# Kernel tuning notes

Hardware: AMD Instinct MI355X
Metric: run time of the kernel (lower is better)

The kernel has to match this reference:

```python
import jax, jax.numpy as jnp
import numpy as np

D_IN, D, N_HEADS, K, VOCAB = 768, 512, 8, 6, 1000
HEAD_DIM = D // N_HEADS


def setup_inputs() -> dict:
    key = jax.random.key(0)
    ks = jax.random.split(key, 16)
    B, T, L = 32, 4096, 512
    s = 0.02
    return {
        "video_features": jax.random.normal(ks[0], (B, T, D_IN), jnp.float32),
        "input_ids": jax.random.randint(ks[1], (B, L), 0, VOCAB),
        "attention_mask": jnp.ones((B, L), jnp.float32),
        # video_encoder (Linear 768->512), stored [in, out]
        "W_enc": jax.random.normal(ks[2], (D_IN, D), jnp.float32) * s,
        "b_enc": jnp.zeros((D,), jnp.float32),
        # frame_selector (Linear 512->1)
        "W_sel": jax.random.normal(ks[3], (D, 1), jnp.float32) * s,
        "b_sel": jnp.zeros((1,), jnp.float32),
        # text_encoder embedding
        "emb": jax.random.normal(ks[4], (VOCAB, D), jnp.float32) * s,
        # MultiheadAttention in/out projections
        "W_q": jax.random.normal(ks[5], (D, D), jnp.float32) * s,
        "W_k": jax.random.normal(ks[6], (D, D), jnp.float32) * s,
        "W_v": jax.random.normal(ks[7], (D, D), jnp.float32) * s,
        "b_q": jnp.zeros((D,), jnp.float32),
        "b_k": jnp.zeros((D,), jnp.float32),
        "b_v": jnp.zeros((D,), jnp.float32),
        "W_o": jax.random.normal(ks[8], (D, D), jnp.float32) * s,
        "b_o": jnp.zeros((D,), jnp.float32),
        # classifier (Linear 512->1000)
        "W_cls": jax.random.normal(ks[9], (D, VOCAB), jnp.float32) * s,
        "b_cls": jnp.zeros((VOCAB,), jnp.float32),
    }


def reference(video_features, input_ids, attention_mask, W_enc, b_enc, W_sel,
              b_sel, emb, W_q, W_k, W_v, b_q, b_k, b_v, W_o, b_o, W_cls, b_cls):
    # encode frames: [B, T, 512]
    ve = jax.nn.relu(jnp.einsum('bti,io->bto', video_features, W_enc) + b_enc)
    # frame scores [B, T] -> top-6 gather
    scores = jnp.einsum('btd,do->bto', ve, W_sel)[..., 0] + b_sel[0]
    _, top_idx = jax.lax.top_k(scores, K)                      # [B, K]
    reps = jnp.take_along_axis(ve, top_idx[:, :, None], axis=1)  # [B, K, 512]
    # text embedding (query), reps as key/value
    txt = emb[input_ids]                                       # [B, L, 512]
    B, L, _ = txt.shape
    q = (txt @ W_q + b_q).reshape(B, L, N_HEADS, HEAD_DIM)
    k = (reps @ W_k + b_k).reshape(B, K, N_HEADS, HEAD_DIM)
    v = (reps @ W_v + b_v).reshape(B, K, N_HEADS, HEAD_DIM)
    scale = 1.0 / np.sqrt(HEAD_DIM).astype(np.float32)
    attn = jax.nn.softmax(jnp.einsum('blhd,bkhd->bhlk', q, k) * scale, axis=-1)
    ctx = jnp.einsum('bhlk,bkhd->blhd', attn, v).reshape(B, L, D)
    fused = ctx @ W_o + b_o
    logits = fused @ W_cls + b_cls                             # [B, L, 1000]
    return logits, reps
```

## Files before the change

### kernel.cpp

```cpp
#include <hip/hip_runtime.h>
#include <math.h>


#define DEV __device__ __forceinline__

typedef _Float16 half8 __attribute__((ext_vector_type(8)));
typedef float f32x4v __attribute__((ext_vector_type(4)));

DEV unsigned short f2h_bits(float f) {
  union { _Float16 h; unsigned short u; } cv;
  cv.h = (_Float16)f;
  return cv.u;
}

DEV void gload16(const void* g, void* lds) {
  auto* gp = reinterpret_cast<const __attribute__((address_space(1))) unsigned int*>(
      reinterpret_cast<unsigned long long>(g));
  auto* lp = reinterpret_cast<__attribute__((address_space(3))) unsigned int*>(
      reinterpret_cast<unsigned long long>(lds));
  __builtin_amdgcn_global_load_lds(gp, lp, 16, 0, 0);
}

__global__ __launch_bounds__(256) void prep_k(
    const float* __restrict__ W_enc, unsigned short* __restrict__ WencT,
    const float* __restrict__ emb, const float* __restrict__ W_q,
    const float* __restrict__ b_q, float* __restrict__ Qe,
    const float* __restrict__ W_o, const float* __restrict__ W_cls,
    unsigned short* __restrict__ WocT, const float* __restrict__ b_o,
    const float* __restrict__ b_cls, float* __restrict__ boc) {
  __shared__ float plds[2080];
  const int blk = blockIdx.x, tid = threadIdx.x;
  if (blk < 96) {
    unsigned short* t = (unsigned short*)plds;
    const int k0 = (blk % 12) * 64, n0 = (blk / 12) * 64;
    for (int e = tid; e < 4096; e += 256) {
      int kk = e >> 6, nn = e & 63;
      t[kk * 65 + nn] = f2h_bits(W_enc[(size_t)(k0 + kk) * 512 + n0 + nn]);
    }
    __syncthreads();
    for (int e = tid; e < 4096; e += 256) {
      int nn = e >> 6, kk = e & 63;
      WencT[(size_t)(n0 + nn) * 768 + k0 + kk] = t[kk * 65 + nn];
    }
  } else if (blk < 346) {
    float* er = plds;
    const int r0 = (blk - 96) * 4;
    for (int i = tid; i < 2048; i += 256) er[i] = emb[(size_t)r0 * 512 + i];
    __syncthreads();
    const int j0 = tid, j1 = tid + 256;
    float a0[4], a1[4];
#pragma unroll
    for (int r = 0; r < 4; ++r) { a0[r] = 0.f; a1[r] = 0.f; }
    for (int i = 0; i < 512; ++i) {
      float w0 = W_q[i * 512 + j0], w1 = W_q[i * 512 + j1];
#pragma unroll
      for (int r = 0; r < 4; ++r) {
        a0[r] += er[r * 512 + i] * w0;
        a1[r] += er[r * 512 + i] * w1;
      }
    }
    float bq0 = b_q[j0], bq1 = b_q[j1];
#pragma unroll
    for (int r = 0; r < 4; ++r) {
      Qe[(size_t)(r0 + r) * 512 + j0] = a0[r] + bq0;
      Qe[(size_t)(r0 + r) * 512 + j1] = a1[r] + bq1;
    }
  } else if (blk < 474) {
    float* wr = plds;
    const int i0 = (blk - 346) * 4;
    for (int i = tid; i < 2048; i += 256) wr[i] = W_o[(size_t)i0 * 512 + i];
    __syncthreads();
    float a[4][4];
#pragma unroll
    for (int r = 0; r < 4; ++r)
#pragma unroll
      for (int c = 0; c < 4; ++c) a[r][c] = 0.f;
    for (int m = 0; m < 512; ++m) {
      float wc[4];
#pragma unroll
      for (int c = 0; c < 4; ++c) {
        int j = tid + c * 256;
        wc[c] = (j < 1000) ? W_cls[(size_t)m * 1000 + j] : 0.f;
      }
#pragma unroll
      for (int r = 0; r < 4; ++r) {
        float x = wr[r * 512 + m];
#pragma unroll
        for (int c = 0; c < 4; ++c) a[r][c] += x * wc[c];
      }
    }
#pragma unroll
    for (int r = 0; r < 4; ++r)
#pragma unroll
      for (int c = 0; c < 4; ++c) {
        int j = tid + c * 256;
        if (j < 1000) WocT[(size_t)j * 512 + i0 + r] = f2h_bits(a[r][c]);
      }
    if (blk == 346) {
      for (int i = tid; i < 24 * 512; i += 256) WocT[512000 + i] = 0;
    }
  } else {
    int j = (blk - 474) * 256 + tid;
    float s = 0.f;
    if (j < 1000) {
      for (int m = 0; m < 512; ++m) s += b_o[m] * W_cls[(size_t)m * 1000 + j];
      s += b_cls[j];
    }
    boc[j] = s;
  }
}

__global__ __launch_bounds__(1024, 4) void score_gemm(
    const float* __restrict__ vf, const unsigned short* __restrict__ WencT,
    const float* __restrict__ b_enc, const float* __restrict__ W_sel,
    const float* __restrict__ b_sel, float* __restrict__ scores) {
  __shared__ unsigned short As[2][128 * 32];
  __shared__ unsigned short Bs[2][512 * 32];
  __shared__ float red[16 * 64];

  const int tid = threadIdx.x;
  const int wv = tid >> 6, lane = tid & 63;
  const int quad = lane >> 4, l15 = lane & 15;
  const int wr = wv >> 3, wc = wv & 7;
  const int rowBase = blockIdx.x * 128;
  const int rso = ((quad ^ (l15 & 3)) << 4);
  char* const AsB0 = (char*)As[0];
  char* const AsB1 = (char*)As[1];
  char* const BsB0 = (char*)Bs[0];
  char* const BsB1 = (char*)Bs[1];

  f32x4v acc[4][4];
#pragma unroll
  for (int i = 0; i < 4; ++i)
#pragma unroll
    for (int j = 0; j < 4; ++j) acc[i][j] = (f32x4v){0.f, 0.f, 0.f, 0.f};

  const int arow = tid >> 3, aseg = tid & 7;
  const float* aSrc = vf + (size_t)(rowBase + arow) * 768 + aseg * 4;
  const int aslot = aseg >> 1, ahalf = aseg & 1;
  const int adst = arow * 64 + ((aslot ^ (arow & 3)) << 4) + ahalf * 8;

  auto packA = [&](float4 f, char* An) {
    uint2 pk;
    pk.x = (unsigned int)f2h_bits(f.x) | ((unsigned int)f2h_bits(f.y) << 16);
    pk.y = (unsigned int)f2h_bits(f.z) | ((unsigned int)f2h_bits(f.w) << 16);
    *(uint2*)(An + adst) = pk;
  };
  auto stage_b = [&](int kk, char* dstB) {
#pragma unroll
    for (int it = 0; it < 2; ++it) {
      int q = tid + it * 1024;
      int n = q >> 2, seg = q & 3;
      gload16(WencT + (size_t)n * 768 + kk * 32 + ((seg ^ (n & 3)) << 3),
              dstB + (it * 1024 + wv * 64) * 16);
    }
  };
  auto consume = [&](const char* A, const char* B) {
    half8 af[4], bf[4];
#pragma unroll
    for (int i = 0; i < 4; ++i) {
      int row = wr * 64 + 16 * i + l15;
      af[i] = *(const half8*)(A + row * 64 + rso);
    }
#pragma unroll
    for (int j = 0; j < 4; ++j) {
      int n = wc * 64 + 16 * j + l15;
      bf[j] = *(const half8*)(B + n * 64 + rso);
    }
#pragma unroll
    for (int i = 0; i < 4; ++i)
#pragma unroll
      for (int j = 0; j < 4; ++j)
        acc[i][j] = __builtin_amdgcn_mfma_f32_16x16x32_f16(af[i], bf[j], acc[i][j], 0, 0, 0);
  };

  stage_b(0, BsB0);
  packA(*(const float4*)(aSrc), AsB0);
  __syncthreads();
  int cur = 0;
  for (int kk = 0; kk < 23; ++kk) {
    float4 fa = *(const float4*)(aSrc + (kk + 1) * 32);
    char* An = cur ? AsB0 : AsB1;
    char* Bn = cur ? BsB0 : BsB1;
    stage_b(kk + 1, Bn);
    consume(cur ? AsB1 : AsB0, cur ? BsB1 : BsB0);
    packA(fa, An);
    __syncthreads();
    cur ^= 1;
  }
  consume(cur ? AsB1 : AsB0, cur ? BsB1 : BsB0);

  float be[4], wsv[4];
#pragma unroll
  for (int j = 0; j < 4; ++j) {
    int col = wc * 64 + 16 * j + l15;
    be[j] = b_enc[col];
    wsv[j] = W_sel[col];
  }
  float part[16];
#pragma unroll
  for (int x = 0; x < 16; ++x) part[x] = 0.f;
#pragma unroll
  for (int i = 0; i < 4; ++i)
#pragma unroll
    for (int j = 0; j < 4; ++j)
#pragma unroll
      for (int r = 0; r < 4; ++r) {
        float v = acc[i][j][r] + be[j];
        v = fmaxf(v, 0.f);
        part[i * 4 + r] += v * wsv[j];
      }
#pragma unroll
  for (int m = 1; m < 16; m <<= 1)
#pragma unroll
    for (int x = 0; x < 16; ++x) part[x] += __shfl_xor(part[x], m);
  if (l15 == 0) {
#pragma unroll
    for (int i = 0; i < 4; ++i)
#pragma unroll
      for (int r = 0; r < 4; ++r)
        red[wv * 64 + 16 * i + quad * 4 + r] = part[i * 4 + r];
  }
  __syncthreads();
  if (tid < 128) {
    const int rh = tid >> 6, rl = tid & 63;
    float s = 0.f;
#pragma unroll
    for (int ww = 0; ww < 8; ++ww) s += red[(rh * 8 + ww) * 64 + rl];
    scores[rowBase + tid] = s + b_sel[0];
  }
}

__global__ __launch_bounds__(256) void topk16(const float* __restrict__ scores,
                                              int* __restrict__ cand) {
  __shared__ float swv[4];
  __shared__ int swi[4];
  __shared__ int winner;
  const int b = blockIdx.x, tid = threadIdx.x;
  const int lane = tid & 63, w = tid >> 6;
  float v[16];
#pragma unroll
  for (int p = 0; p < 16; ++p) v[p] = scores[b * 4096 + p * 256 + tid];
  for (int r = 0; r < 16; ++r) {
    float bv = v[0];
    int bp = 0;
#pragma unroll
    for (int p = 1; p < 16; ++p)
      if (v[p] > bv) { bv = v[p]; bp = p; }
    int bi = bp * 256 + tid;
#pragma unroll
    for (int m = 1; m < 64; m <<= 1) {
      float ov = __shfl_xor(bv, m);
      int oi = __shfl_xor(bi, m);
      if (ov > bv || (ov == bv && oi < bi)) { bv = ov; bi = oi; }
    }
    if (lane == 0) { swv[w] = bv; swi[w] = bi; }
    __syncthreads();
    if (tid == 0) {
      float fv = swv[0];
      int fi = swi[0];
#pragma unroll
      for (int x = 1; x < 4; ++x)
        if (swv[x] > fv || (swv[x] == fv && swi[x] < fi)) { fv = swv[x]; fi = swi[x]; }
      cand[b * 16 + r] = fi;
      winner = fi;
    }
    __syncthreads();
    const int wi = winner;
    const int wp = wi >> 8, wt = wi & 255;
#pragma unroll
    for (int p = 0; p < 16; ++p)
      if (p == wp && tid == wt) v[p] = -3.0e38f;
    __syncthreads();
  }
}

__global__ __launch_bounds__(256) void rescore(
    const float* __restrict__ vf, const int* __restrict__ cand,
    const float* __restrict__ W_enc, const float* __restrict__ b_enc,
    const float* __restrict__ W_sel, const float* __restrict__ b_sel,
    float* __restrict__ veC, float* __restrict__ exsc) {
  __shared__ float vfs[4][768];
  __shared__ float redl[16];
  const int b = blockIdx.x, cb = blockIdx.y * 4, tid = threadIdx.x;
  for (int c = 0; c < 4; ++c) {
    int t = cand[b * 16 + cb + c];
    const float* src = vf + ((size_t)b * 4096 + t) * 768;
    for (int i = tid; i < 768; i += 256) vfs[c][i] = src[i];
  }
  __syncthreads();
  const int j0 = tid, j1 = tid + 256;
  float a0[4] = {0.f, 0.f, 0.f, 0.f}, a1[4] = {0.f, 0.f, 0.f, 0.f};
  for (int i = 0; i < 768; ++i) {
    float w0 = W_enc[(size_t)i * 512 + j0], w1 = W_enc[(size_t)i * 512 + j1];
#pragma unroll
    for (int c = 0; c < 4; ++c) {
      float x = vfs[c][i];
      a0[c] += x * w0;
      a1[c] += x * w1;
    }
  }
  float ws0 = W_sel[j0], ws1 = W_sel[j1];
  float be0 = b_enc[j0], be1 = b_enc[j1];
  float s[4];
#pragma unroll
  for (int c = 0; c < 4; ++c) {
    float v0 = fmaxf(a0[c] + be0, 0.f);
    float v1 = fmaxf(a1[c] + be1, 0.f);
    veC[((size_t)b * 16 + cb + c) * 512 + j0] = v0;
    veC[((size_t)b * 16 + cb + c) * 512 + j1] = v1;
    s[c] = v0 * ws0 + v1 * ws1;
  }
#pragma unroll
  for (int m = 1; m < 64; m <<= 1)
#pragma unroll
    for (int c = 0; c < 4; ++c) s[c] += __shfl_xor(s[c], m);
  int w = tid >> 6;
  if ((tid & 63) == 0) {
#pragma unroll
    for (int c = 0; c < 4; ++c) redl[c * 4 + w] = s[c];
  }
  __syncthreads();
  if (tid < 4)
    exsc[b * 16 + cb + tid] = redl[tid * 4 + 0] + redl[tid * 4 + 1] +
                              redl[tid * 4 + 2] + redl[tid * 4 + 3] + b_sel[0];
}

__global__ __launch_bounds__(256) void select6(
    const float* __restrict__ exsc, const int* __restrict__ cand,
    const float* __restrict__ veC, int* __restrict__ sel,
    float* __restrict__ repsOut) {
  __shared__ int selL[6];
  const int b = blockIdx.x, tid = threadIdx.x;
  if (tid == 0) {
    float v[16]; int idx[16]; bool used[16];
    for (int c = 0; c < 16; ++c) {
      v[c] = exsc[b * 16 + c];
      idx[c] = cand[b * 16 + c];
      used[c] = false;
    }
    for (int r = 0; r < 6; ++r) {
      int bi = -1;
      for (int c = 0; c < 16; ++c) {
        if (used[c]) continue;
        if (bi < 0 || v[c] > v[bi] || (v[c] == v[bi] && idx[c] < idx[bi])) bi = c;
      }
      used[bi] = true;
      selL[r] = bi;
      sel[b * 6 + r] = bi;
    }
  }
  __syncthreads();
  for (int r = 0; r < 6; ++r) {
    int c = selL[r];
    for (int i = tid; i < 512; i += 256)
      repsOut[((size_t)b * 6 + r) * 512 + i] = veC[((size_t)b * 16 + c) * 512 + i];
  }
}

__global__ __launch_bounds__(256) void kv_proj(
    const int* __restrict__ sel, const float* __restrict__ veC,
    const float* __restrict__ W_k, const float* __restrict__ W_v,
    const float* __restrict__ b_k, const float* __restrict__ b_v,
    float* __restrict__ Ks, float* __restrict__ Vs) {
  __shared__ float rep[512];
  const int br = blockIdx.x;
  const int b = br / 6;
  const int tid = threadIdx.x;
  const int c = sel[br];
  for (int i = tid; i < 512; i += 256) rep[i] = veC[((size_t)b * 16 + c) * 512 + i];
  __syncthreads();
  const int j0 = tid, j1 = tid + 256;
  float k0 = 0.f, k1 = 0.f, v0 = 0.f, v1 = 0.f;
  for (int m = 0; m < 512; ++m) {
    float x = rep[m];
    k0 += x * W_k[m * 512 + j0];
    k1 += x * W_k[m * 512 + j1];
    v0 += x * W_v[m * 512 + j0];
    v1 += x * W_v[m * 512 + j1];
  }
  Ks[(size_t)br * 512 + j0] = (k0 + b_k[j0]) * 0.125f;
  Ks[(size_t)br * 512 + j1] = (k1 + b_k[j1]) * 0.125f;
  Vs[(size_t)br * 512 + j0] = v0 + b_v[j0];
  Vs[(size_t)br * 512 + j1] = v1 + b_v[j1];
}

__global__ __launch_bounds__(256) void ctx_kernel(
    const int* __restrict__ ids, const float* __restrict__ Qe,
    const float* __restrict__ Ks, const float* __restrict__ Vs,
    unsigned short* __restrict__ CTX) {
  const int token = blockIdx.x * 4 + (threadIdx.x >> 6);
  const int lane = threadIdx.x & 63;
  const int b = token >> 9;
  const int id = ids[token];
  float q[8];
#pragma unroll
  for (int h = 0; h < 8; ++h) q[h] = Qe[(size_t)id * 512 + h * 64 + lane];
  float s[8][6];
#pragma unroll
  for (int kk = 0; kk < 6; ++kk) {
    const float* kp = Ks + ((size_t)b * 6 + kk) * 512 + lane;
    float p[8];
#pragma unroll
    for (int h = 0; h < 8; ++h) p[h] = q[h] * kp[h * 64];
#pragma unroll
    for (int m = 1; m < 64; m <<= 1)
#pragma unroll
      for (int h = 0; h < 8; ++h) p[h] += __shfl_xor(p[h], m);
#pragma unroll
    for (int h = 0; h < 8; ++h) s[h][kk] = p[h];
  }
  const float* vbase = Vs + (size_t)b * 6 * 512 + lane;
#pragma unroll
  for (int h = 0; h < 8; ++h) {
    float mx = s[h][0];
#pragma unroll
    for (int kk = 1; kk < 6; ++kk) mx = fmaxf(mx, s[h][kk]);
    float e[6], sum = 0.f;
#pragma unroll
    for (int kk = 0; kk < 6; ++kk) { e[kk] = __expf(s[h][kk] - mx); sum += e[kk]; }
    float c = 0.f;
#pragma unroll
    for (int kk = 0; kk < 6; ++kk) c += e[kk] * vbase[(size_t)kk * 512 + h * 64];
    c *= (1.f / sum);
    CTX[(size_t)token * 512 + h * 64 + lane] = f2h_bits(c);
  }
}

__global__ __launch_bounds__(1024, 4) void logits_gemm(
    const unsigned short* __restrict__ CTX, const unsigned short* __restrict__ WocT,
    const float* __restrict__ boc, float* __restrict__ out) {
  __shared__ unsigned short As[2][128 * 32];
  __shared__ unsigned short Bs[2][512 * 32];
  const int tid = threadIdx.x;
  const int wv = tid >> 6, lane = tid & 63;
  const int quad = lane >> 4, l15 = lane & 15;
  const int wr = wv >> 3, wc = wv & 7;
  const int rowBase = blockIdx.x * 128;
  const int n0 = blockIdx.y * 512;
  const int rso = ((quad ^ (l15 & 3)) << 4);
  char* const AsB0 = (char*)As[0];
  char* const AsB1 = (char*)As[1];
  char* const BsB0 = (char*)Bs[0];
  char* const BsB1 = (char*)Bs[1];

  f32x4v acc[4][4];
#pragma unroll
  for (int i = 0; i < 4; ++i)
#pragma unroll
    for (int j = 0; j < 4; ++j) acc[i][j] = (f32x4v){0.f, 0.f, 0.f, 0.f};

  const int arow = tid >> 2, aseg = tid & 3;

  auto stage = [&](int kk, char* An, char* Bn) {
    const int k0 = kk * 32;
    if (wv < 8) {
      gload16(CTX + (size_t)(rowBase + arow) * 512 + k0 + ((aseg ^ (arow & 3)) << 3),
              An + wv * 1024);
    }
#pragma unroll
    for (int it = 0; it < 2; ++it) {
      int q = tid + it * 1024;
      int n = q >> 2, seg = q & 3;
      gload16(WocT + (size_t)(n0 + n) * 512 + k0 + ((seg ^ (n & 3)) << 3),
              Bn + (it * 1024 + wv * 64) * 16);
    }
  };
  auto consume = [&](const char* A, const char* B) {
    half8 af[4], bf[4];
#pragma unroll
    for (int i = 0; i < 4; ++i) {
      int row = wr * 64 + 16 * i + l15;
      af[i] = *(const half8*)(A + row * 64 + rso);
    }
#pragma unroll
    for (int j = 0; j < 4; ++j) {
      int n = wc * 64 + 16 * j + l15;
      bf[j] = *(const half8*)(B + n * 64 + rso);
    }
#pragma unroll
    for (int i = 0; i < 4; ++i)
#pragma unroll
      for (int j = 0; j < 4; ++j)
        acc[i][j] = __builtin_amdgcn_mfma_f32_16x16x32_f16(af[i], bf[j], acc[i][j], 0, 0, 0);
  };

  stage(0, AsB0, BsB0);
  __syncthreads();
  int cur = 0;
  for (int kk = 0; kk < 15; ++kk) {
    stage(kk + 1, cur ? AsB0 : AsB1, cur ? BsB0 : BsB1);
    consume(cur ? AsB1 : AsB0, cur ? BsB1 : BsB0);
    __syncthreads();
    cur ^= 1;
  }
  consume(cur ? AsB1 : AsB0, cur ? BsB1 : BsB0);

  float bo[4];
#pragma unroll
  for (int j = 0; j < 4; ++j) bo[j] = boc[n0 + wc * 64 + 16 * j + l15];
#pragma unroll
  for (int i = 0; i < 4; ++i)
#pragma unroll
    for (int j = 0; j < 4; ++j)
#pragma unroll
      for (int r = 0; r < 4; ++r) {
        int token = rowBase + wr * 64 + 16 * i + quad * 4 + r;
        int col = n0 + wc * 64 + 16 * j + l15;
        if (col < 1000) out[(size_t)token * 1000 + col] = acc[i][j][r] + bo[j];
      }
}

extern "C" void kernel_launch(void* const* d_in, const int* in_sizes, int n_in,
                              void* d_out, int out_size, void* d_ws, size_t ws_size,
                              hipStream_t stream) {
  (void)in_sizes; (void)n_in; (void)out_size; (void)ws_size;
  const float* vf    = (const float*)d_in[0];
  const int*   ids   = (const int*)d_in[1];
  const float* W_enc = (const float*)d_in[3];
  const float* b_enc = (const float*)d_in[4];
  const float* W_sel = (const float*)d_in[5];
  const float* b_sel = (const float*)d_in[6];
  const float* emb   = (const float*)d_in[7];
  const float* W_q   = (const float*)d_in[8];
  const float* W_k   = (const float*)d_in[9];
  const float* W_v   = (const float*)d_in[10];
  const float* b_q   = (const float*)d_in[11];
  const float* b_k   = (const float*)d_in[12];
  const float* b_v   = (const float*)d_in[13];
  const float* W_o   = (const float*)d_in[14];
  const float* b_o   = (const float*)d_in[15];
  const float* W_cls = (const float*)d_in[16];
  const float* b_cls = (const float*)d_in[17];

  float* out = (float*)d_out;
  float* reps_out = out + (size_t)16384000;

  char* p = (char*)d_ws;
  auto nxt = [&](size_t bytes) -> char* {
    char* q = p;
    p += (bytes + 255) & ~(size_t)255;
    return q;
  };
  unsigned short* WencT = (unsigned short*)nxt((size_t)512 * 768 * 2);
  unsigned short* WocT  = (unsigned short*)nxt((size_t)1024 * 512 * 2);
  unsigned short* CTX   = (unsigned short*)nxt((size_t)16384 * 512 * 2);
  float* scores = (float*)nxt((size_t)131072 * 4);
  int*   cand   = (int*)nxt((size_t)512 * 4);
  float* exsc   = (float*)nxt((size_t)512 * 4);
  float* veC    = (float*)nxt((size_t)32 * 16 * 512 * 4);
  int*   sel    = (int*)nxt((size_t)192 * 4);
  float* Ks     = (float*)nxt((size_t)98304 * 4);
  float* Vs     = (float*)nxt((size_t)98304 * 4);
  float* Qe     = (float*)nxt((size_t)512000 * 4);
  float* boc    = (float*)nxt((size_t)1024 * 4);

  hipLaunchKernelGGL(prep_k,      dim3(478),    dim3(256), 0, stream,
                     W_enc, WencT, emb, W_q, b_q, Qe, W_o, W_cls, WocT, b_o, b_cls, boc);
  hipLaunchKernelGGL(score_gemm,  dim3(1024),   dim3(1024), 0, stream,
                     vf, WencT, b_enc, W_sel, b_sel, scores);
  hipLaunchKernelGGL(topk16,      dim3(32),     dim3(256), 0, stream, scores, cand);
  hipLaunchKernelGGL(rescore,     dim3(32, 4),  dim3(256), 0, stream,
                     vf, cand, W_enc, b_enc, W_sel, b_sel, veC, exsc);
  hipLaunchKernelGGL(select6,     dim3(32),     dim3(256), 0, stream, exsc, cand, veC, sel, reps_out);
  hipLaunchKernelGGL(kv_proj,     dim3(192),    dim3(256), 0, stream, sel, veC, W_k, W_v, b_k, b_v, Ks, Vs);
  hipLaunchKernelGGL(ctx_kernel,  dim3(4096),   dim3(256), 0, stream, ids, Qe, Ks, Vs, CTX);
  hipLaunchKernelGGL(logits_gemm, dim3(128, 2), dim3(1024), 0, stream, CTX, WocT, boc, out);
}
```

Baseline: 976.6 us.

## Shrink GEMM blocks to 4 waves with 64-row tiles and wider per-wave N

Both the score GEMM and the logits GEMM move from 1024-thread blocks with 128-row tiles to 256-thread blocks with 64-row tiles. Each wave now covers 64x128 outputs with 32 accumulators instead of 64x64, and the grid doubles. The intent is higher occupancy and more blocks per CU, with more MFMA work per LDS fragment load. In exchange, the B tile (512x32) is loaded by half as many rows of A, so B traffic per output doubles and register pressure rises.

```diff
diff --git a/kernel.cpp b/kernel.cpp
--- a/kernel.cpp
+++ b/kernel.cpp
@@ -110,123 +110,134 @@
   }
 }
 
-__global__ __launch_bounds__(1024, 4) void score_gemm(
+__global__ __launch_bounds__(256, 2) void score_gemm(
     const float* __restrict__ vf, const unsigned short* __restrict__ WencT,
     const float* __restrict__ b_enc, const float* __restrict__ W_sel,
     const float* __restrict__ b_sel, float* __restrict__ scores) {
-  __shared__ unsigned short As[2][128 * 32];
+  __shared__ unsigned short As[2][64 * 32];
   __shared__ unsigned short Bs[2][512 * 32];
-  __shared__ float red[16 * 64];
+  __shared__ float red[8 * 64];
 
   const int tid = threadIdx.x;
   const int wv = tid >> 6, lane = tid & 63;
   const int quad = lane >> 4, l15 = lane & 15;
-  const int wr = wv >> 3, wc = wv & 7;
-  const int rowBase = blockIdx.x * 128;
+  const int rowBase = blockIdx.x * 64;
   const int rso = ((quad ^ (l15 & 3)) << 4);
   char* const AsB0 = (char*)As[0];
   char* const AsB1 = (char*)As[1];
   char* const BsB0 = (char*)Bs[0];
   char* const BsB1 = (char*)Bs[1];
 
-  f32x4v acc[4][4];
+  f32x4v acc[4][8];
 #pragma unroll
   for (int i = 0; i < 4; ++i)
 #pragma unroll
-    for (int j = 0; j < 4; ++j) acc[i][j] = (f32x4v){0.f, 0.f, 0.f, 0.f};
-
-  const int arow = tid >> 3, aseg = tid & 7;
-  const float* aSrc = vf + (size_t)(rowBase + arow) * 768 + aseg * 4;
-  const int aslot = aseg >> 1, ahalf = aseg & 1;
-  const int adst = arow * 64 + ((aslot ^ (arow & 3)) << 4) + ahalf * 8;
-
-  auto packA = [&](float4 f, char* An) {
-    uint2 pk;
-    pk.x = (unsigned int)f2h_bits(f.x) | ((unsigned int)f2h_bits(f.y) << 16);
-    pk.y = (unsigned int)f2h_bits(f.z) | ((unsigned int)f2h_bits(f.w) << 16);
-    *(uint2*)(An + adst) = pk;
+    for (int j = 0; j < 8; ++j) acc[i][j] = (f32x4v){0.f, 0.f, 0.f, 0.f};
+
+  const int arow = tid >> 2, aseg = tid & 3;
+  const float* aSrc = vf + (size_t)(rowBase + arow) * 768 + aseg * 8;
+  const int adst = arow * 64 + ((aseg ^ (arow & 3)) << 4);
+
+  auto packA = [&](float4 fa, float4 fb, char* An) {
+    uint4 pk;
+    pk.x = (unsigned int)f2h_bits(fa.x) | ((unsigned int)f2h_bits(fa.y) << 16);
+    pk.y = (unsigned int)f2h_bits(fa.z) | ((unsigned int)f2h_bits(fa.w) << 16);
+    pk.z = (unsigned int)f2h_bits(fb.x) | ((unsigned int)f2h_bits(fb.y) << 16);
+    pk.w = (unsigned int)f2h_bits(fb.z) | ((unsigned int)f2h_bits(fb.w) << 16);
+    *(uint4*)(An + adst) = pk;
   };
   auto stage_b = [&](int kk, char* dstB) {
 #pragma unroll
-    for (int it = 0; it < 2; ++it) {
-      int q = tid + it * 1024;
+    for (int it = 0; it < 8; ++it) {
+      int q = tid + it * 256;
       int n = q >> 2, seg = q & 3;
       gload16(WencT + (size_t)n * 768 + kk * 32 + ((seg ^ (n & 3)) << 3),
-              dstB + (it * 1024 + wv * 64) * 16);
+              dstB + (it * 256 + wv * 64) * 16);
     }
   };
   auto consume = [&](const char* A, const char* B) {
-    half8 af[4], bf[4];
+    half8 af[4], bf[8];
 #pragma unroll
     for (int i = 0; i < 4; ++i) {
-      int row = wr * 64 + 16 * i + l15;
+      int row = 16 * i + l15;
       af[i] = *(const half8*)(A + row * 64 + rso);
     }
 #pragma unroll
-    for (int j = 0; j < 4; ++j) {
-      int n = wc * 64 + 16 * j + l15;
+    for (int j = 0; j < 8; ++j) {
+      int n = wv * 128 + 16 * j + l15;
       bf[j] = *(const half8*)(B + n * 64 + rso);
     }
 #pragma unroll
     for (int i = 0; i < 4; ++i)
 #pragma unroll
-      for (int j = 0; j < 4; ++j)
+      for (int j = 0; j < 8; ++j)
         acc[i][j] = __builtin_amdgcn_mfma_f32_16x16x32_f16(af[i], bf[j], acc[i][j], 0, 0, 0);
   };
 
   stage_b(0, BsB0);
-  packA(*(const float4*)(aSrc), AsB0);
+  {
+    float4 fa = *(const float4*)(aSrc);
+    float4 fb = *(const float4*)(aSrc + 4);
+    packA(fa, fb, AsB0);
+  }
   __syncthreads();
   int cur = 0;
   for (int kk = 0; kk < 23; ++kk) {
-    float4 fa = *(const float4*)(aSrc + (kk + 1) * 32);
+    const float* s = aSrc + (kk + 1) * 32;
+    float4 fa = *(const float4*)(s);
+    float4 fb = *(const float4*)(s + 4);
     char* An = cur ? AsB0 : AsB1;
     char* Bn = cur ? BsB0 : BsB1;
     stage_b(kk + 1, Bn);
     consume(cur ? AsB1 : AsB0, cur ? BsB1 : BsB0);
-    packA(fa, An);
+    packA(fa, fb, An);
     __syncthreads();
     cur ^= 1;
   }
   consume(cur ? AsB1 : AsB0, cur ? BsB1 : BsB0);
 
-  float be[4], wsv[4];
-#pragma unroll
-  for (int j = 0; j < 4; ++j) {
-    int col = wc * 64 + 16 * j + l15;
+  float be[8], wsv[8];
+#pragma unroll
+  for (int j = 0; j < 8; ++j) {
+    int col = wv * 128 + 16 * j + l15;
     be[j] = b_enc[col];
     wsv[j] = W_sel[col];
   }
-  float part[16];
-#pragma unroll
-  for (int x = 0; x < 16; ++x) part[x] = 0.f;
+  float plo[16], phi[16];
+#pragma unroll
+  for (int x = 0; x < 16; ++x) { plo[x] = 0.f; phi[x] = 0.f; }
 #pragma unroll
   for (int i = 0; i < 4; ++i)
 #pragma unroll
-    for (int j = 0; j < 4; ++j)
+    for (int j = 0; j < 8; ++j)
 #pragma unroll
       for (int r = 0; r < 4; ++r) {
         float v = acc[i][j][r] + be[j];
         v = fmaxf(v, 0.f);
-        part[i * 4 + r] += v * wsv[j];
+        if (j < 4) plo[i * 4 + r] += v * wsv[j];
+        else       phi[i * 4 + r] += v * wsv[j];
       }
 #pragma unroll
   for (int m = 1; m < 16; m <<= 1)
 #pragma unroll
-    for (int x = 0; x < 16; ++x) part[x] += __shfl_xor(part[x], m);
+    for (int x = 0; x < 16; ++x) {
+      plo[x] += __shfl_xor(plo[x], m);
+      phi[x] += __shfl_xor(phi[x], m);
+    }
   if (l15 == 0) {
 #pragma unroll
     for (int i = 0; i < 4; ++i)
 #pragma unroll
-      for (int r = 0; r < 4; ++r)
-        red[wv * 64 + 16 * i + quad * 4 + r] = part[i * 4 + r];
-  }
-  __syncthreads();
-  if (tid < 128) {
-    const int rh = tid >> 6, rl = tid & 63;
+      for (int r = 0; r < 4; ++r) {
+        red[(2 * wv + 0) * 64 + 16 * i + quad * 4 + r] = plo[i * 4 + r];
+        red[(2 * wv + 1) * 64 + 16 * i + quad * 4 + r] = phi[i * 4 + r];
+      }
+  }
+  __syncthreads();
+  if (tid < 64) {
     float s = 0.f;
 #pragma unroll
-    for (int ww = 0; ww < 8; ++ww) s += red[(rh * 8 + ww) * 64 + rl];
+    for (int ww = 0; ww < 8; ++ww) s += red[ww * 64 + tid];
     scores[rowBase + tid] = s + b_sel[0];
   }
 }
@@ -427,16 +438,15 @@
   }
 }
 
-__global__ __launch_bounds__(1024, 4) void logits_gemm(
+__global__ __launch_bounds__(256, 2) void logits_gemm(
     const unsigned short* __restrict__ CTX, const unsigned short* __restrict__ WocT,
     const float* __restrict__ boc, float* __restrict__ out) {
-  __shared__ unsigned short As[2][128 * 32];
+  __shared__ unsigned short As[2][64 * 32];
   __shared__ unsigned short Bs[2][512 * 32];
   const int tid = threadIdx.x;
   const int wv = tid >> 6, lane = tid & 63;
   const int quad = lane >> 4, l15 = lane & 15;
-  const int wr = wv >> 3, wc = wv & 7;
-  const int rowBase = blockIdx.x * 128;
+  const int rowBase = blockIdx.x * 64;
   const int n0 = blockIdx.y * 512;
   const int rso = ((quad ^ (l15 & 3)) << 4);
   char* const AsB0 = (char*)As[0];
@@ -444,44 +454,42 @@
   char* const BsB0 = (char*)Bs[0];
   char* const BsB1 = (char*)Bs[1];
 
-  f32x4v acc[4][4];
+  f32x4v acc[4][8];
 #pragma unroll
   for (int i = 0; i < 4; ++i)
 #pragma unroll
-    for (int j = 0; j < 4; ++j) acc[i][j] = (f32x4v){0.f, 0.f, 0.f, 0.f};
+    for (int j = 0; j < 8; ++j) acc[i][j] = (f32x4v){0.f, 0.f, 0.f, 0.f};
 
   const int arow = tid >> 2, aseg = tid & 3;
 
   auto stage = [&](int kk, char* An, char* Bn) {
     const int k0 = kk * 32;
-    if (wv < 8) {
-      gload16(CTX + (size_t)(rowBase + arow) * 512 + k0 + ((aseg ^ (arow & 3)) << 3),
-              An + wv * 1024);
-    }
-#pragma unroll
-    for (int it = 0; it < 2; ++it) {
-      int q = tid + it * 1024;
+    gload16(CTX + (size_t)(rowBase + arow) * 512 + k0 + ((aseg ^ (arow & 3)) << 3),
+            An + wv * 1024);
+#pragma unroll
+    for (int it = 0; it < 8; ++it) {
+      int q = tid + it * 256;
       int n = q >> 2, seg = q & 3;
       gload16(WocT + (size_t)(n0 + n) * 512 + k0 + ((seg ^ (n & 3)) << 3),
-              Bn + (it * 1024 + wv * 64) * 16);
+              Bn + (it * 256 + wv * 64) * 16);
     }
   };
   auto consume = [&](const char* A, const char* B) {
-    half8 af[4], bf[4];
+    half8 af[4], bf[8];
 #pragma unroll
     for (int i = 0; i < 4; ++i) {
-      int row = wr * 64 + 16 * i + l15;
+      int row = 16 * i + l15;
       af[i] = *(const half8*)(A + row * 64 + rso);
     }
 #pragma unroll
-    for (int j = 0; j < 4; ++j) {
-      int n = wc * 64 + 16 * j + l15;
+    for (int j = 0; j < 8; ++j) {
+      int n = wv * 128 + 16 * j + l15;
       bf[j] = *(const half8*)(B + n * 64 + rso);
     }
 #pragma unroll
     for (int i = 0; i < 4; ++i)
 #pragma unroll
-      for (int j = 0; j < 4; ++j)
+      for (int j = 0; j < 8; ++j)
         acc[i][j] = __builtin_amdgcn_mfma_f32_16x16x32_f16(af[i], bf[j], acc[i][j], 0, 0, 0);
   };
 
@@ -496,17 +504,17 @@
   }
   consume(cur ? AsB1 : AsB0, cur ? BsB1 : BsB0);
 
-  float bo[4];
-#pragma unroll
-  for (int j = 0; j < 4; ++j) bo[j] = boc[n0 + wc * 64 + 16 * j + l15];
+  float bo[8];
+#pragma unroll
+  for (int j = 0; j < 8; ++j) bo[j] = boc[n0 + wv * 128 + 16 * j + l15];
 #pragma unroll
   for (int i = 0; i < 4; ++i)
 #pragma unroll
-    for (int j = 0; j < 4; ++j)
+    for (int j = 0; j < 8; ++j)
 #pragma unroll
       for (int r = 0; r < 4; ++r) {
-        int token = rowBase + wr * 64 + 16 * i + quad * 4 + r;
-        int col = n0 + wc * 64 + 16 * j + l15;
+        int token = rowBase + 16 * i + quad * 4 + r;
+        int col = n0 + wv * 128 + 16 * j + l15;
         if (col < 1000) out[(size_t)token * 1000 + col] = acc[i][j][r] + bo[j];
       }
 }
@@ -557,7 +565,7 @@
 
   hipLaunchKernelGGL(prep_k,      dim3(478),    dim3(256), 0, stream,
                      W_enc, WencT, emb, W_q, b_q, Qe, W_o, W_cls, WocT, b_o, b_cls, boc);
-  hipLaunchKernelGGL(score_gemm,  dim3(1024),   dim3(1024), 0, stream,
+  hipLaunchKernelGGL(score_gemm,  dim3(2048),   dim3(256), 0, stream,
                      vf, WencT, b_enc, W_sel, b_sel, scores);
   hipLaunchKernelGGL(topk16,      dim3(32),     dim3(256), 0, stream, scores, cand);
   hipLaunchKernelGGL(rescore,     dim3(32, 4),  dim3(256), 0, stream,
@@ -565,5 +573,5 @@
   hipLaunchKernelGGL(select6,     dim3(32),     dim3(256), 0, stream, exsc, cand, veC, sel, reps_out);
   hipLaunchKernelGGL(kv_proj,     dim3(192),    dim3(256), 0, stream, sel, veC, W_k, W_v, b_k, b_v, Ks, Vs);
   hipLaunchKernelGGL(ctx_kernel,  dim3(4096),   dim3(256), 0, stream, ids, Qe, Ks, Vs, CTX);
-  hipLaunchKernelGGL(logits_gemm, dim3(128, 2), dim3(1024), 0, stream, CTX, WocT, boc, out);
-}
+  hipLaunchKernelGGL(logits_gemm, dim3(256, 2), dim3(256), 0, stream, CTX, WocT, boc, out);
+}
```

Measured after the change: 1.018 ms. 4.3% more time.

## Pre-swizzle weights into MFMA fragment layout and load B directly from global

Applied to the files above, without the earlier changes.

The prep kernel now writes the fp16 W_enc and the fused W_o·W_cls weights in a per-fragment layout that matches the MFMA B-operand lane order. Both GEMMs then read B fragments straight from global/L2 into registers instead of staging them through LDS, which removes the B LDS buffers and their traffic. The trade-off is that every wave issues repeated global loads of B that were previously shared through LDS, so the GEMMs lean on cache bandwidth and latency. Separately, select6 and kv_proj are merged into one kernel that recomputes the rank selection per block, removing one launch.

```diff
diff --git a/kernel.cpp b/kernel.cpp
--- a/kernel.cpp
+++ b/kernel.cpp
@@ -22,11 +22,11 @@
 }
 
 __global__ __launch_bounds__(256) void prep_k(
-    const float* __restrict__ W_enc, unsigned short* __restrict__ WencT,
+    const float* __restrict__ W_enc, unsigned short* __restrict__ WencF,
     const float* __restrict__ emb, const float* __restrict__ W_q,
     const float* __restrict__ b_q, float* __restrict__ Qe,
     const float* __restrict__ W_o, const float* __restrict__ W_cls,
-    unsigned short* __restrict__ WocT, const float* __restrict__ b_o,
+    unsigned short* __restrict__ WocF, const float* __restrict__ b_o,
     const float* __restrict__ b_cls, float* __restrict__ boc) {
   __shared__ float plds[2080];
   const int blk = blockIdx.x, tid = threadIdx.x;
@@ -39,8 +39,11 @@
     }
     __syncthreads();
     for (int e = tid; e < 4096; e += 256) {
-      int nn = e >> 6, kk = e & 63;
-      WencT[(size_t)(n0 + nn) * 768 + k0 + kk] = t[kk * 65 + nn];
+      int frag = e >> 9, within = e & 511;
+      int n0g = frag >> 1, kg = frag & 1;
+      int quad = within >> 7, l15 = (within >> 3) & 15, ki = within & 7;
+      WencF[(size_t)(((n0 >> 4) + n0g) * 24 + (k0 >> 5) + kg) * 512 + within] =
+          t[(kg * 32 + quad * 8 + ki) * 65 + n0g * 16 + l15];
     }
   } else if (blk < 346) {
     float* er = plds;
@@ -94,10 +97,17 @@
 #pragma unroll
       for (int c = 0; c < 4; ++c) {
         int j = tid + c * 256;
-        if (j < 1000) WocT[(size_t)j * 512 + i0 + r] = f2h_bits(a[r][c]);
+        int k = i0 + r;
+        if (j < 1000)
+          WocF[(size_t)((j >> 4) * 16 + (k >> 5)) * 512 +
+               (((k >> 3) & 3) << 7) + ((j & 15) << 3) + (k & 7)] = f2h_bits(a[r][c]);
       }
     if (blk == 346) {
-      for (int i = tid; i < 24 * 512; i += 256) WocT[512000 + i] = 0;
+      for (int e = tid; e < 24 * 512; e += 256) {
+        int n = 1000 + (e >> 9), k = e & 511;
+        WocF[(size_t)((n >> 4) * 16 + (k >> 5)) * 512 +
+             (((k >> 3) & 3) << 7) + ((n & 15) << 3) + (k & 7)] = 0;
+      }
     }
   } else {
     int j = (blk - 474) * 256 + tid;
@@ -111,11 +121,10 @@
 }
 
 __global__ __launch_bounds__(1024, 4) void score_gemm(
-    const float* __restrict__ vf, const unsigned short* __restrict__ WencT,
+    const float* __restrict__ vf, const unsigned short* __restrict__ WencF,
     const float* __restrict__ b_enc, const float* __restrict__ W_sel,
     const float* __restrict__ b_sel, float* __restrict__ scores) {
   __shared__ unsigned short As[2][128 * 32];
-  __shared__ unsigned short Bs[2][512 * 32];
   __shared__ float red[16 * 64];
 
   const int tid = threadIdx.x;
@@ -126,8 +135,6 @@
   const int rso = ((quad ^ (l15 & 3)) << 4);
   char* const AsB0 = (char*)As[0];
   char* const AsB1 = (char*)As[1];
-  char* const BsB0 = (char*)Bs[0];
-  char* const BsB1 = (char*)Bs[1];
 
   f32x4v acc[4][4];
 #pragma unroll
@@ -146,49 +153,36 @@
     pk.y = (unsigned int)f2h_bits(f.z) | ((unsigned int)f2h_bits(f.w) << 16);
     *(uint2*)(An + adst) = pk;
   };
-  auto stage_b = [&](int kk, char* dstB) {
-#pragma unroll
-    for (int it = 0; it < 2; ++it) {
-      int q = tid + it * 1024;
-      int n = q >> 2, seg = q & 3;
-      gload16(WencT + (size_t)n * 768 + kk * 32 + ((seg ^ (n & 3)) << 3),
-              dstB + (it * 1024 + wv * 64) * 16);
-    }
-  };
-  auto consume = [&](const char* A, const char* B) {
+  const unsigned short* const bBase = WencF + (size_t)lane * 8;
+  auto consume = [&](const char* A, int kk) {
     half8 af[4], bf[4];
+#pragma unroll
+    for (int j = 0; j < 4; ++j)
+      bf[j] = *(const half8*)(bBase + (size_t)((wc * 4 + j) * 24 + kk) * 512);
 #pragma unroll
     for (int i = 0; i < 4; ++i) {
       int row = wr * 64 + 16 * i + l15;
       af[i] = *(const half8*)(A + row * 64 + rso);
     }
 #pragma unroll
-    for (int j = 0; j < 4; ++j) {
-      int n = wc * 64 + 16 * j + l15;
-      bf[j] = *(const half8*)(B + n * 64 + rso);
-    }
-#pragma unroll
     for (int i = 0; i < 4; ++i)
 #pragma unroll
       for (int j = 0; j < 4; ++j)
         acc[i][j] = __builtin_amdgcn_mfma_f32_16x16x32_f16(af[i], bf[j], acc[i][j], 0, 0, 0);
   };
 
-  stage_b(0, BsB0);
   packA(*(const float4*)(aSrc), AsB0);
   __syncthreads();
   int cur = 0;
   for (int kk = 0; kk < 23; ++kk) {
     float4 fa = *(const float4*)(aSrc + (kk + 1) * 32);
     char* An = cur ? AsB0 : AsB1;
-    char* Bn = cur ? BsB0 : BsB1;
-    stage_b(kk + 1, Bn);
-    consume(cur ? AsB1 : AsB0, cur ? BsB1 : BsB0);
+    consume(cur ? AsB1 : AsB0, kk);
     packA(fa, An);
     __syncthreads();
     cur ^= 1;
   }
-  consume(cur ? AsB1 : AsB0, cur ? BsB1 : BsB0);
+  consume(cur ? AsB1 : AsB0, 23);
 
   float be[4], wsv[4];
 #pragma unroll
@@ -326,12 +320,17 @@
                               redl[tid * 4 + 2] + redl[tid * 4 + 3] + b_sel[0];
 }
 
-__global__ __launch_bounds__(256) void select6(
+__global__ __launch_bounds__(256) void selkv_k(
     const float* __restrict__ exsc, const int* __restrict__ cand,
-    const float* __restrict__ veC, int* __restrict__ sel,
-    float* __restrict__ repsOut) {
-  __shared__ int selL[6];
-  const int b = blockIdx.x, tid = threadIdx.x;
+    const float* __restrict__ veC, const float* __restrict__ W_k,
+    const float* __restrict__ W_v, const float* __restrict__ b_k,
+    const float* __restrict__ b_v, float* __restrict__ repsOut,
+    float* __restrict__ Ks, float* __restrict__ Vs) {
+  __shared__ float rep[512];
+  __shared__ int selc;
+  const int br = blockIdx.x;
+  const int b = br / 6, rk = br - b * 6;
+  const int tid = threadIdx.x;
   if (tid == 0) {
     float v[16]; int idx[16]; bool used[16];
     for (int c = 0; c < 16; ++c) {
@@ -339,36 +338,24 @@
       idx[c] = cand[b * 16 + c];
       used[c] = false;
     }
-    for (int r = 0; r < 6; ++r) {
-      int bi = -1;
+    int bi = -1;
+    for (int r = 0; r <= rk; ++r) {
+      bi = -1;
       for (int c = 0; c < 16; ++c) {
         if (used[c]) continue;
         if (bi < 0 || v[c] > v[bi] || (v[c] == v[bi] && idx[c] < idx[bi])) bi = c;
       }
       used[bi] = true;
-      selL[r] = bi;
-      sel[b * 6 + r] = bi;
-    }
-  }
-  __syncthreads();
-  for (int r = 0; r < 6; ++r) {
-    int c = selL[r];
-    for (int i = tid; i < 512; i += 256)
-      repsOut[((size_t)b * 6 + r) * 512 + i] = veC[((size_t)b * 16 + c) * 512 + i];
-  }
-}
-
-__global__ __launch_bounds__(256) void kv_proj(
-    const int* __restrict__ sel, const float* __restrict__ veC,
-    const float* __restrict__ W_k, const float* __restrict__ W_v,
-    const float* __restrict__ b_k, const float* __restrict__ b_v,
-    float* __restrict__ Ks, float* __restrict__ Vs) {
-  __shared__ float rep[512];
-  const int br = blockIdx.x;
-  const int b = br / 6;
-  const int tid = threadIdx.x;
-  const int c = sel[br];
-  for (int i = tid; i < 512; i += 256) rep[i] = veC[((size_t)b * 16 + c) * 512 + i];
+    }
+    selc = bi;
+  }
+  __syncthreads();
+  const int c = selc;
+  for (int i = tid; i < 512; i += 256) {
+    float x = veC[((size_t)b * 16 + c) * 512 + i];
+    repsOut[((size_t)b * 6 + rk) * 512 + i] = x;
+    rep[i] = x;
+  }
   __syncthreads();
   const int j0 = tid, j1 = tid + 256;
   float k0 = 0.f, k1 = 0.f, v0 = 0.f, v1 = 0.f;
@@ -428,10 +415,9 @@
 }
 
 __global__ __launch_bounds__(1024, 4) void logits_gemm(
-    const unsigned short* __restrict__ CTX, const unsigned short* __restrict__ WocT,
+    const unsigned short* __restrict__ CTX, const unsigned short* __restrict__ WocF,
     const float* __restrict__ boc, float* __restrict__ out) {
   __shared__ unsigned short As[2][128 * 32];
-  __shared__ unsigned short Bs[2][512 * 32];
   const int tid = threadIdx.x;
   const int wv = tid >> 6, lane = tid & 63;
   const int quad = lane >> 4, l15 = lane & 15;
@@ -441,8 +427,6 @@
   const int rso = ((quad ^ (l15 & 3)) << 4);
   char* const AsB0 = (char*)As[0];
   char* const AsB1 = (char*)As[1];
-  char* const BsB0 = (char*)Bs[0];
-  char* const BsB1 = (char*)Bs[1];
 
   f32x4v acc[4][4];
 #pragma unroll
@@ -452,49 +436,42 @@
 
   const int arow = tid >> 2, aseg = tid & 3;
 
-  auto stage = [&](int kk, char* An, char* Bn) {
+  auto stageA = [&](int kk, char* An) {
     const int k0 = kk * 32;
     if (wv < 8) {
       gload16(CTX + (size_t)(rowBase + arow) * 512 + k0 + ((aseg ^ (arow & 3)) << 3),
               An + wv * 1024);
     }
-#pragma unroll
-    for (int it = 0; it < 2; ++it) {
-      int q = tid + it * 1024;
-      int n = q >> 2, seg = q & 3;
-      gload16(WocT + (size_t)(n0 + n) * 512 + k0 + ((seg ^ (n & 3)) << 3),
-              Bn + (it * 1024 + wv * 64) * 16);
-    }
   };
-  auto consume = [&](const char* A, const char* B) {
+  const unsigned short* const bBase = WocF + (size_t)lane * 8;
+  const int nG = (n0 >> 4) + wc * 4;
+  auto consume = [&](const char* A, int kk) {
     half8 af[4], bf[4];
+#pragma unroll
+    for (int j = 0; j < 4; ++j)
+      bf[j] = *(const half8*)(bBase + (size_t)((nG + j) * 16 + kk) * 512);
 #pragma unroll
     for (int i = 0; i < 4; ++i) {
       int row = wr * 64 + 16 * i + l15;
       af[i] = *(const half8*)(A + row * 64 + rso);
     }
 #pragma unroll
-    for (int j = 0; j < 4; ++j) {
-      int n = wc * 64 + 16 * j + l15;
-      bf[j] = *(const half8*)(B + n * 64 + rso);
-    }
-#pragma unroll
     for (int i = 0; i < 4; ++i)
 #pragma unroll
       for (int j = 0; j < 4; ++j)
         acc[i][j] = __builtin_amdgcn_mfma_f32_16x16x32_f16(af[i], bf[j], acc[i][j], 0, 0, 0);
   };
 
-  stage(0, AsB0, BsB0);
+  stageA(0, AsB0);
   __syncthreads();
   int cur = 0;
   for (int kk = 0; kk < 15; ++kk) {
-    stage(kk + 1, cur ? AsB0 : AsB1, cur ? BsB0 : BsB1);
-    consume(cur ? AsB1 : AsB0, cur ? BsB1 : BsB0);
+    stageA(kk + 1, cur ? AsB0 : AsB1);
+    consume(cur ? AsB1 : AsB0, kk);
     __syncthreads();
     cur ^= 1;
   }
-  consume(cur ? AsB1 : AsB0, cur ? BsB1 : BsB0);
+  consume(cur ? AsB1 : AsB0, 15);
 
   float bo[4];
 #pragma unroll
@@ -542,28 +519,27 @@
     p += (bytes + 255) & ~(size_t)255;
     return q;
   };
-  unsigned short* WencT = (unsigned short*)nxt((size_t)512 * 768 * 2);
-  unsigned short* WocT  = (unsigned short*)nxt((size_t)1024 * 512 * 2);
+  unsigned short* WencF = (unsigned short*)nxt((size_t)512 * 768 * 2);
+  unsigned short* WocF  = (unsigned short*)nxt((size_t)1024 * 512 * 2);
   unsigned short* CTX   = (unsigned short*)nxt((size_t)16384 * 512 * 2);
   float* scores = (float*)nxt((size_t)131072 * 4);
   int*   cand   = (int*)nxt((size_t)512 * 4);
   float* exsc   = (float*)nxt((size_t)512 * 4);
   float* veC    = (float*)nxt((size_t)32 * 16 * 512 * 4);
-  int*   sel    = (int*)nxt((size_t)192 * 4);
   float* Ks     = (float*)nxt((size_t)98304 * 4);
   float* Vs     = (float*)nxt((size_t)98304 * 4);
   float* Qe     = (float*)nxt((size_t)512000 * 4);
   float* boc    = (float*)nxt((size_t)1024 * 4);
 
   hipLaunchKernelGGL(prep_k,      dim3(478),    dim3(256), 0, stream,
-                     W_enc, WencT, emb, W_q, b_q, Qe, W_o, W_cls, WocT, b_o, b_cls, boc);
+                     W_enc, WencF, emb, W_q, b_q, Qe, W_o, W_cls, WocF, b_o, b_cls, boc);
   hipLaunchKernelGGL(score_gemm,  dim3(1024),   dim3(1024), 0, stream,
-                     vf, WencT, b_enc, W_sel, b_sel, scores);
+                     vf, WencF, b_enc, W_sel, b_sel, scores);
   hipLaunchKernelGGL(topk16,      dim3(32),     dim3(256), 0, stream, scores, cand);
   hipLaunchKernelGGL(rescore,     dim3(32, 4),  dim3(256), 0, stream,
                      vf, cand, W_enc, b_enc, W_sel, b_sel, veC, exsc);
-  hipLaunchKernelGGL(select6,     dim3(32),     dim3(256), 0, stream, exsc, cand, veC, sel, reps_out);
-  hipLaunchKernelGGL(kv_proj,     dim3(192),    dim3(256), 0, stream, sel, veC, W_k, W_v, b_k, b_v, Ks, Vs);
+  hipLaunchKernelGGL(selkv_k,     dim3(192),    dim3(256), 0, stream,
+                     exsc, cand, veC, W_k, W_v, b_k, b_v, reps_out, Ks, Vs);
   hipLaunchKernelGGL(ctx_kernel,  dim3(4096),   dim3(256), 0, stream, ids, Qe, Ks, Vs, CTX);
-  hipLaunchKernelGGL(logits_gemm, dim3(128, 2), dim3(1024), 0, stream, CTX, WocT, boc, out);
-}
+  hipLaunchKernelGGL(logits_gemm, dim3(128, 2), dim3(1024), 0, stream, CTX, WocF, boc, out);
+}
```

Measured after the change: 985.2 us. No clear change (+0.9%).
